# Optimization experiments

Measured on AMD Instinct MI355X. Metric: run time of the kernel, lower is better.

## Reference

```python
import jax, jax.numpy as jnp
import numpy as np

B, T, C = 2, 2048, 2048
HK, HV, DK, DV, KW = 16, 32, 128, 128, 4
KEY_DIM = HK * DK          # 2048
VAL_DIM = HV * DV          # 4096
QKV_DIM = 2 * KEY_DIM + VAL_DIM  # 8192
REPEAT = HV // HK
EPS = 1e-6


def setup_inputs() -> dict:
    key = jax.random.key(0)
    ks = jax.random.split(key, 12)
    s = 0.02
    return {
        "x": jax.random.normal(ks[0], (B, T, C), jnp.float32),
        "positions": jnp.arange(B * T, dtype=jnp.int64).reshape(B, T) % T,
        "W_qkv": jax.random.normal(ks[1], (QKV_DIM, C), jnp.float32) * s,
        "W_z": jax.random.normal(ks[2], (VAL_DIM, C), jnp.float32) * s,
        "W_b": jax.random.normal(ks[3], (HV, C), jnp.float32) * s,
        "W_a": jax.random.normal(ks[4], (HV, C), jnp.float32) * s,
        "conv_w": jax.random.normal(ks[5], (QKV_DIM, 1, KW), jnp.float32) * 0.3,
        "dt_bias": jnp.ones((HV,), jnp.float32),
        "A_log": jnp.log(jax.random.uniform(ks[6], (HV,), jnp.float32, 0.01, 16.0)),
        "norm_w": jnp.ones((DV,), jnp.float32),
        "W_out": jax.random.normal(ks[7], (C, VAL_DIM), jnp.float32) * s,
    }


def _forward(x, W_qkv, W_z, W_b, W_a, conv_w, dt_bias, A_log, norm_w, W_out):
    qkv = x @ W_qkv.T                                # [B,T,QKV_DIM]
    z = (x @ W_z.T).reshape(B, T, HV, DV)
    b = x @ W_b.T                                    # [B,T,HV]
    a = x @ W_a.T                                    # [B,T,HV]

    # depthwise causal conv1d (left pad KW-1), then SiLU
    qkv_c = jnp.transpose(qkv, (0, 2, 1))            # [B,QKV_DIM,T]
    qkv_c = jax.lax.conv_general_dilated(
        qkv_c, conv_w, window_strides=(1,), padding=[(KW - 1, 0)],
        dimension_numbers=("NCH", "OIH", "NCH"), feature_group_count=QKV_DIM)
    qkv = jax.nn.silu(jnp.transpose(qkv_c, (0, 2, 1)))

    q, k, v = jnp.split(qkv, [KEY_DIM, 2 * KEY_DIM], axis=-1)
    q = q.reshape(B, T, HK, DK)
    k = k.reshape(B, T, HK, DK)
    v = v.reshape(B, T, HV, DV)
    q = q / jnp.maximum(jnp.linalg.norm(q, axis=-1, keepdims=True), 1e-12)
    k = k / jnp.maximum(jnp.linalg.norm(k, axis=-1, keepdims=True), 1e-12)
    if REPEAT > 1:
        q = jnp.repeat(q, REPEAT, axis=2)            # [B,T,HV,DK]
        k = jnp.repeat(k, REPEAT, axis=2)

    beta = jax.nn.sigmoid(b)                         # [B,T,HV]
    g = -jnp.exp(A_log) * jax.nn.softplus(a + dt_bias)  # [B,T,HV]

    # gated delta-rule recurrence over time (lax.scan, time-major)
    def step(state, inp):
        g_t, beta_t, k_t, v_t, q_t = inp             # [B,HV], [B,HV], [B,HV,DK], [B,HV,DV], [B,HV,DK]
        state = jnp.exp(g_t)[..., None, None] * state \
            + beta_t[..., None, None] * (k_t[..., :, None] * v_t[..., None, :])
        out_t = jnp.einsum("bhk,bhkv->bhv", q_t, state)
        return state, out_t

    tm = lambda u: jnp.moveaxis(u, 1, 0)
    state0 = jnp.zeros((B, HV, DK, DV), x.dtype)
    _, out = jax.lax.scan(step, state0, (tm(g), tm(beta), tm(k), tm(v), tm(q)))
    out = jnp.moveaxis(out, 0, 1)                    # [B,T,HV,DV]

    # gated RMSNorm per head: RMSNorm(out) * silu(z)
    o = out.astype(jnp.float32)
    o = o * jax.lax.rsqrt(jnp.mean(o * o, axis=-1, keepdims=True) + EPS)
    o = (norm_w * o) * jax.nn.silu(z.astype(jnp.float32))
    o = o.astype(x.dtype).reshape(B, T, VAL_DIM)
    return o @ W_out.T                               # [B,T,C]


def reference(x, positions, W_qkv, W_z, W_b, W_a, conv_w, dt_bias, A_log, norm_w, W_out):
    del positions  # unused by the module's math
    return _forward(x, W_qkv, W_z, W_b, W_a, conv_w, dt_bias, A_log, norm_w, W_out)
```

## Files before the change

### kernel.cpp

```cpp
#include <hip/hip_runtime.h>

typedef unsigned short u16;
typedef unsigned int u32;
typedef __attribute__((ext_vector_type(8))) short short8;
typedef __attribute__((ext_vector_type(8))) _Float16 half8;
typedef __attribute__((ext_vector_type(4))) float f32x4;

#define NB 2
#define NT 2048
#define NC 2048
#define NHV 32
#define VALD 4096
#define NBT 4096
#define CL 64
#define NCH (NT / CL)

#define GL16(gp, lp) __builtin_amdgcn_global_load_lds( \
    (const __attribute__((address_space(1))) unsigned int*)(gp), \
    (__attribute__((address_space(3))) unsigned int*)(lp), 16, 0, 0)

static __device__ __forceinline__ float bf2f(u16 u) {
  union { u32 u; float f; } x; x.u = ((u32)u) << 16; return x.f;
}
static __device__ __forceinline__ u16 f2bf(float f) {
  union { float f; u32 u; } x; x.f = f;
  u32 r = x.u + 0x7fffu + ((x.u >> 16) & 1u);
  return (u16)(r >> 16);
}
static __device__ __forceinline__ u16 f2h(float f) {
  union { _Float16 h; u16 u; } c; c.h = (_Float16)f; return c.u;
}
static __device__ __forceinline__ float h2f(u16 u) {
  union { u16 u; _Float16 h; } c; c.u = u; return (float)c.h;
}
static __device__ __forceinline__ float sigm(float x) { return 1.0f / (1.0f + __expf(-x)); }
static __device__ __forceinline__ int ldsoff(int row, int c8) {
  return row * 48 + ((c8 ^ ((row >> 2) & 3)) << 3);
}

__global__ void k_sentinel(float* out) { out[0] = 1.0e6f; }

__global__ __launch_bounds__(256) void k_cvtx(const float* __restrict__ in, u16* __restrict__ hi,
                                              u16* __restrict__ lo, u16* __restrict__ h16, int n4) {
  int i = blockIdx.x * 256 + threadIdx.x;
  if (i >= n4) return;
  float4 v = ((const float4*)in)[i];
  ushort4 h, l, p;
  h.x = f2bf(v.x); l.x = f2bf(v.x - bf2f(h.x)); p.x = f2h(v.x);
  h.y = f2bf(v.y); l.y = f2bf(v.y - bf2f(h.y)); p.y = f2h(v.y);
  h.z = f2bf(v.z); l.z = f2bf(v.z - bf2f(h.z)); p.z = f2h(v.z);
  h.w = f2bf(v.w); l.w = f2bf(v.w - bf2f(h.w)); p.w = f2h(v.w);
  ((ushort4*)hi)[i] = h;
  ((ushort4*)lo)[i] = l;
  ((ushort4*)h16)[i] = p;
}

__global__ __launch_bounds__(256) void k_cvt16(const float* __restrict__ in, u16* __restrict__ out, int n4) {
  int i = blockIdx.x * 256 + threadIdx.x;
  if (i >= n4) return;
  float4 v = ((const float4*)in)[i];
  ushort4 o;
  o.x = f2h(v.x); o.y = f2h(v.y); o.z = f2h(v.z); o.w = f2h(v.w);
  ((ushort4*)out)[i] = o;
}

__global__ __launch_bounds__(256) void k_wba(const float* __restrict__ Wb, const float* __restrict__ Wa,
                                             u16* __restrict__ hi, u16* __restrict__ lo) {
  int i = blockIdx.x * 256 + threadIdx.x;
  int r = i >> 11, c = i & 2047;
  float v = 0.f;
  if (r < 32) v = Wb[r * 2048 + c];
  else if (r < 64) v = Wa[(r - 32) * 2048 + c];
  u16 h = f2bf(v);
  hi[i] = h;
  lo[i] = f2bf(v - bf2f(h));
}

__global__ __launch_bounds__(256) void k_gemm_bf3(const u16* __restrict__ Ahg, const u16* __restrict__ Alg,
                                                  const u16* __restrict__ Bhg, const u16* __restrict__ Blg,
                                                  float* __restrict__ C0, int M, int N, int K) {
  __shared__ __align__(16) u16 As_h[128 * 48];
  __shared__ __align__(16) u16 As_l[128 * 48];
  __shared__ __align__(16) u16 Bs_h[128 * 48];
  __shared__ __align__(16) u16 Bs_l[128 * 48];
  const int tid = threadIdx.x;
  const int lane = tid & 63, wave = tid >> 6;
  const int wr = wave >> 1, wc = wave & 1;
  const int l15 = lane & 15, l16 = lane >> 4;
  const int row0 = blockIdx.y * 128, col0 = blockIdx.x * 128;
  const int sr = tid >> 1, sk = (tid & 1) * 16;
  const int c0 = sk >> 3;
  const int w0 = ldsoff(sr, c0), w1 = ldsoff(sr, c0 + 1);
  f32x4 acc[4][4] = {};
  for (int k0 = 0; k0 < K; k0 += 32) {
    const size_t aoff = (size_t)(row0 + sr) * K + k0 + sk;
    const size_t boff = (size_t)(col0 + sr) * K + k0 + sk;
    *(short8*)&As_h[w0] = *(const short8*)&Ahg[aoff];
    *(short8*)&As_h[w1] = *(const short8*)&Ahg[aoff + 8];
    *(short8*)&As_l[w0] = *(const short8*)&Alg[aoff];
    *(short8*)&As_l[w1] = *(const short8*)&Alg[aoff + 8];
    *(short8*)&Bs_h[w0] = *(const short8*)&Bhg[boff];
    *(short8*)&Bs_h[w1] = *(const short8*)&Bhg[boff + 8];
    *(short8*)&Bs_l[w0] = *(const short8*)&Blg[boff];
    *(short8*)&Bs_l[w1] = *(const short8*)&Blg[boff + 8];
    __syncthreads();
    short8 ah[4], al[4], bh[4], bl[4];
#pragma unroll
    for (int mi = 0; mi < 4; ++mi) {
      int off = ldsoff(wr * 64 + mi * 16 + l15, l16);
      ah[mi] = *(short8*)&As_h[off];
      al[mi] = *(short8*)&As_l[off];
    }
#pragma unroll
    for (int ni = 0; ni < 4; ++ni) {
      int off = ldsoff(wc * 64 + ni * 16 + l15, l16);
      bh[ni] = *(short8*)&Bs_h[off];
      bl[ni] = *(short8*)&Bs_l[off];
    }
#pragma unroll
    for (int mi = 0; mi < 4; ++mi)
#pragma unroll
      for (int ni = 0; ni < 4; ++ni) {
        acc[mi][ni] = __builtin_amdgcn_mfma_f32_16x16x32_bf16(ah[mi], bh[ni], acc[mi][ni], 0, 0, 0);
        acc[mi][ni] = __builtin_amdgcn_mfma_f32_16x16x32_bf16(al[mi], bh[ni], acc[mi][ni], 0, 0, 0);
        acc[mi][ni] = __builtin_amdgcn_mfma_f32_16x16x32_bf16(ah[mi], bl[ni], acc[mi][ni], 0, 0, 0);
      }
    __syncthreads();
  }
#pragma unroll
  for (int mi = 0; mi < 4; ++mi)
#pragma unroll
    for (int ni = 0; ni < 4; ++ni) {
      int rr = row0 + wr * 64 + mi * 16 + l16 * 4;
      int cc = col0 + wc * 64 + ni * 16 + l15;
#pragma unroll
      for (int i = 0; i < 4; ++i)
        C0[(size_t)(rr + i) * N + cc] = acc[mi][ni][i];
    }
}

template <int MODE>
__global__ __launch_bounds__(256) void k_gemm16(const u16* __restrict__ Ag, const u16* __restrict__ Bg,
                                                void* __restrict__ C0, int M, int N, int K,
                                                const u16* __restrict__ e0, const float* __restrict__ e1,
                                                const float* __restrict__ e2) {
  __shared__ __align__(16) u16 As[2 * 128 * 64];
  __shared__ __align__(16) u16 Bs[2 * 128 * 64];
  const int tid = threadIdx.x;
  const int lane = tid & 63, wave = tid >> 6;
  const int wr = wave >> 1, wc = wave & 1;
  const int l15 = lane & 15, l16 = lane >> 4;
  const int qx = gridDim.x >> 3;
  const int swz = ((int)blockIdx.x & 7) * qx + ((int)blockIdx.x >> 3);
  const int nbx = N >> 7;
  const int row0 = (swz / nbx) * 128, col0 = (swz % nbx) * 128;
  u32 gA[4], gB[4], lofs[4];
#pragma unroll
  for (int i = 0; i < 4; ++i) {
    int o = wave * 2048 + i * 512 + lane * 8;
    int row = o >> 6;
    int cg = ((lane & 7) ^ (row & 7)) * 8;
    gA[i] = (u32)(row0 + row) * (u32)K + cg;
    gB[i] = (u32)(col0 + row) * (u32)K + cg;
    lofs[i] = (u32)(wave * 2048 + i * 512);
  }
  f32x4 acc[4][4] = {};
  const int NTILE = K >> 6;
#pragma unroll
  for (int i = 0; i < 4; ++i) {
    GL16(Ag + gA[i], &As[lofs[i]]);
    GL16(Bg + gB[i], &Bs[lofs[i]]);
  }
  for (int t = 0; t < NTILE; ++t) {
    const u32 cb = (u32)(t & 1) * 8192;
    __syncthreads();
    if (t + 1 < NTILE) {
      const u32 nb = cb ^ 8192;
      const int kn = (t + 1) << 6;
#pragma unroll
      for (int i = 0; i < 4; ++i) {
        GL16(Ag + gA[i] + kn, &As[nb + lofs[i]]);
        GL16(Bg + gB[i] + kn, &Bs[nb + lofs[i]]);
      }
    }
#pragma unroll
    for (int kk = 0; kk < 2; ++kk) {
      half8 a[4], b[4];
#pragma unroll
      for (int mi = 0; mi < 4; ++mi) {
        int row = wr * 64 + mi * 16 + l15;
        a[mi] = *(half8*)&As[cb + row * 64 + (((kk * 4 + l16) ^ (l15 & 7)) << 3)];
      }
#pragma unroll
      for (int ni = 0; ni < 4; ++ni) {
        int row = wc * 64 + ni * 16 + l15;
        b[ni] = *(half8*)&Bs[cb + row * 64 + (((kk * 4 + l16) ^ (l15 & 7)) << 3)];
      }
#pragma unroll
      for (int mi = 0; mi < 4; ++mi)
#pragma unroll
        for (int ni = 0; ni < 4; ++ni)
          acc[mi][ni] = __builtin_amdgcn_mfma_f32_16x16x32_f16(a[mi], b[ni], acc[mi][ni], 0, 0, 0);
    }
  }
#pragma unroll
  for (int mi = 0; mi < 4; ++mi) {
#pragma unroll
    for (int ni = 0; ni < 4; ++ni) {
      int rr = row0 + wr * 64 + mi * 16 + l16 * 4;
      int cc = col0 + wc * 64 + ni * 16 + l15;
#pragma unroll
      for (int i = 0; i < 4; ++i) {
        float v = acc[mi][ni][i];
        size_t idx = (size_t)(rr + i) * N + cc;
        if constexpr (MODE == 0) {
          ((float*)C0)[idx] = v;
        } else if constexpr (MODE == 1) {
          ((u16*)C0)[idx] = f2h(v);
        } else {
          float zs = v * sigm(v);
          float o = h2f(e0[idx]) * e1[(size_t)(rr + i) * 32 + (cc >> 7)] * e2[cc & 127] * zs;
          ((u16*)C0)[idx] = f2h(o);
        }
      }
    }
  }
}

__global__ __launch_bounds__(256) void k_bg(const float* __restrict__ ba, const float* __restrict__ dt_bias,
                                            const float* __restrict__ A_log, float* __restrict__ beta_t,
                                            float* __restrict__ g_t) {
  int i = blockIdx.x * 256 + threadIdx.x;
  int bt = i >> 5, h = i & 31;
  float bv = ba[(size_t)bt * 128 + h];
  float av = ba[(size_t)bt * 128 + 32 + h];
  beta_t[h * 4096 + bt] = sigm(bv);
  float xx = av + dt_bias[h];
  float sp = (xx > 20.f) ? xx : log1pf(__expf(xx));
  g_t[h * 4096 + bt] = -__expf(A_log[h]) * sp;
}

__global__ __launch_bounds__(256) void k_convqk(const u16* __restrict__ qkraw, const float* __restrict__ cw,
                                                u16* __restrict__ qkn) {
  __shared__ float sval[4096];
  __shared__ float snrm[32];
  const int tid = threadIdx.x;
  const int bt = blockIdx.x;
  const int b = bt >> 11, t = bt & 2047;
  for (int i = 0; i < 16; ++i) {
    int c = i * 256 + tid;
    float acc = 0.f;
#pragma unroll
    for (int j = 0; j < 4; ++j) {
      int ts = t - 3 + j;
      if (ts >= 0) acc += cw[c * 4 + j] * h2f(qkraw[(size_t)(b * 2048 + ts) * 4096 + c]);
    }
    sval[c] = acc * sigm(acc);
  }
  __syncthreads();
  {
    int gidx = tid >> 3, s = tid & 7;
    float ss = 0.f;
#pragma unroll
    for (int i2 = 0; i2 < 16; ++i2) { float v = sval[gidx * 128 + s * 16 + i2]; ss += v * v; }
    ss += __shfl_xor(ss, 1); ss += __shfl_xor(ss, 2); ss += __shfl_xor(ss, 4);
    if (s == 0) snrm[gidx] = 1.0f / fmaxf(sqrtf(ss), 1e-12f);
  }
  __syncthreads();
  for (int i = 0; i < 16; ++i) {
    int c = i * 256 + tid;
    qkn[(size_t)bt * 4096 + c] = f2h(sval[c] * snrm[c >> 7]);
  }
}

__global__ __launch_bounds__(512, 4) void k_scanc(const u16* __restrict__ qk16, const u16* __restrict__ v16,
                                                  const float* __restrict__ cw,
                                                  const float* __restrict__ beta_t, const float* __restrict__ g_t,
                                                  u16* __restrict__ outr) {
  __shared__ __align__(16) u16 Qs[64][136], Ks[64][136];
  __shared__ __align__(16) u16 Vs[32][72];
  __shared__ __align__(16) u16 SIs[64][72];
  __shared__ __align__(16) u16 SH[2][32][132];
  __shared__ u16 rv16[67][36];
  __shared__ float garr[2][64], barr[2][64], warr[2][64], earr[2][64];
  __shared__ float sdt[2];

  const int tid = threadIdx.x;
  const int lane = tid & 63, wv = tid >> 6;
  const int l15 = lane & 15, l16 = lane >> 4;
  const int dq = blockIdx.x & 3, h = (blockIdx.x >> 2) & 31, b = blockIdx.x >> 7;
  const int bT = b * 2048;
  const int hk = h >> 1;
  const int dvl = tid & 31;
  const int vch = h * 128 + dq * 32;
  const float4 cwv = *(const float4*)&cw[(4096 + vch + dvl) * 4];
  const int mblk = wv & 3, nh = wv >> 2;
  const int m0 = mblk * 16;
  const int sr = tid >> 3, d0 = (tid & 7) * 16;
  const int r0v = tid >> 5;

  for (int i = tid; i < 2 * 32 * 132; i += 512) ((u16*)SH)[i] = 0;
  f32x4 st[2] = {};

  short8 pq[2], pk[2];
  u16 pv[5];
  float pgv, pbv;
  auto LOADQK = [&](int t0) {
    const size_t base = (size_t)(bT + t0 + sr) * 4096 + hk * 128 + d0;
    pq[0] = *(const short8*)&qk16[base];        pq[1] = *(const short8*)&qk16[base + 8];
    pk[0] = *(const short8*)&qk16[base + 2048]; pk[1] = *(const short8*)&qk16[base + 2056];
  };
  auto LOADV = [&](int t0) {
#pragma unroll
    for (int i = 0; i < 5; ++i) {
      int r = r0v + i * 16;
      int tr = t0 - 3 + r;
      pv[i] = (r < 67 && tr >= 0) ? v16[(size_t)(bT + tr) * 4096 + vch + dvl] : (u16)0;
    }
  };
  auto CUMSUM = [&](float gv, float bv, int buf) {
    float cum = gv;
#pragma unroll
    for (int off = 1; off < 64; off <<= 1) {
      float o = __shfl_up(cum, off);
      if (lane >= off) cum += o;
    }
    float tot = __shfl(cum, 63);
    garr[buf][lane] = cum;
    earr[buf][lane] = __expf(cum);
    warr[buf][lane] = __expf(tot - cum) * bv;
    barr[buf][lane] = bv;
    if (lane == 0) sdt[buf] = __expf(tot);
  };

  LOADQK(0);
  LOADV(0);
  if (wv == 0) {
    float gv = g_t[h * 4096 + bT + lane];
    float bv = beta_t[h * 4096 + bT + lane];
    CUMSUM(gv, bv, 0);
  }

  for (int ch = 0; ch < NCH; ++ch) {
    const int t0 = ch * CL;
    const int p = ch & 1;
    *(short8*)&Qs[sr][d0] = pq[0]; *(short8*)&Qs[sr][d0 + 8] = pq[1];
    *(short8*)&Ks[sr][d0] = pk[0]; *(short8*)&Ks[sr][d0 + 8] = pk[1];
#pragma unroll
    for (int i = 0; i < 5; ++i) {
      int r = r0v + i * 16;
      if (r < 67) rv16[r][dvl] = pv[i];
    }
    __syncthreads();
    if (ch + 1 < NCH) {
      LOADQK(t0 + CL);
      LOADV(t0 + CL);
      if (wv == 0) {
        pgv = g_t[h * 4096 + bT + t0 + CL + lane];
        pbv = beta_t[h * 4096 + bT + t0 + CL + lane];
      }
    }
    {
      int tl = tid >> 5;
#pragma unroll
      for (int rr = 0; rr < 4; ++rr) {
        int t = rr * 16 + tl;
        float a = cwv.x * h2f(rv16[t][dvl]) + cwv.y * h2f(rv16[t + 1][dvl]) +
                  cwv.z * h2f(rv16[t + 2][dvl]) + cwv.w * h2f(rv16[t + 3][dvl]);
        a = a * sigm(a);
        Vs[dvl][t] = f2h(a);
      }
    }
    half8 a[4];
#pragma unroll
    for (int kk = 0; kk < 4; ++kk) a[kk] = *(half8*)&Qs[m0 + l15][l16 * 8 + kk * 32];
#pragma unroll
    for (int j = 0; j < 2; ++j) {
      int n = nh * 2 + j;
      f32x4 a4 = {};
#pragma unroll
      for (int kk = 0; kk < 4; ++kk) {
        half8 b8 = *(half8*)&Ks[n * 16 + l15][l16 * 8 + kk * 32];
        a4 = __builtin_amdgcn_mfma_f32_16x16x32_f16(a[kk], b8, a4, 0, 0, 0);
      }
      int col = n * 16 + l15;
      float gc = garr[p][col], bc = barr[p][col];
#pragma unroll
      for (int i = 0; i < 4; ++i) {
        int row = m0 + l16 * 4 + i;
        float cval = (col <= row) ? __expf(garr[p][row] - gc) * bc * a4[i] : 0.f;
        SIs[row][col] = f2h(cval);
      }
    }
    __syncthreads();
    f32x4 ao = {};
#pragma unroll
    for (int kk = 0; kk < 4; ++kk) {
      half8 s8 = *(half8*)&SH[p][nh * 16 + l15][l16 * 8 + kk * 32];
      ao = __builtin_amdgcn_mfma_f32_16x16x32_f16(a[kk], s8, ao, 0, 0, 0);
    }
#pragma unroll
    for (int i = 0; i < 4; ++i) ao[i] *= earr[p][m0 + l16 * 4 + i];
#pragma unroll
    for (int kk = 0; kk < 2; ++kk) {
      half8 asi = *(half8*)&SIs[m0 + l15][l16 * 8 + kk * 32];
      half8 bv8 = *(half8*)&Vs[nh * 16 + l15][l16 * 8 + kk * 32];
      ao = __builtin_amdgcn_mfma_f32_16x16x32_f16(asi, bv8, ao, 0, 0, 0);
    }
#pragma unroll
    for (int i = 0; i < 4; ++i)
      outr[(size_t)(bT + t0 + m0 + l16 * 4 + i) * 4096 + vch + nh * 16 + l15] = f2h(ao[i]);
    const float sd = sdt[p];
#pragma unroll
    for (int m = 0; m < 2; ++m)
#pragma unroll
      for (int i = 0; i < 4; ++i) st[m][i] *= sd;
#pragma unroll
    for (int kk = 0; kk < 2; ++kk) {
      half8 bw;
      {
        int dk = wv * 16 + l15;
#pragma unroll
        for (int e = 0; e < 8; ++e) {
          int s = l16 * 8 + e + kk * 32;
          bw[e] = (_Float16)(h2f(Ks[s][dk]) * warr[p][s]);
        }
      }
#pragma unroll
      for (int m = 0; m < 2; ++m) {
        half8 av = *(half8*)&Vs[m * 16 + l15][l16 * 8 + kk * 32];
        st[m] = __builtin_amdgcn_mfma_f32_16x16x32_f16(av, bw, st[m], 0, 0, 0);
      }
    }
#pragma unroll
    for (int m = 0; m < 2; ++m)
#pragma unroll
      for (int i = 0; i < 4; ++i)
        SH[p ^ 1][m * 16 + l16 * 4 + i][wv * 16 + l15] = f2h(st[m][i]);
    if (wv == 0 && ch + 1 < NCH) CUMSUM(pgv, pbv, p ^ 1);
    __syncthreads();
  }
}

__global__ __launch_bounds__(256) void k_rms(const u16* __restrict__ outr, float* __restrict__ rms) {
  int pair = blockIdx.x * 4 + (threadIdx.x >> 6);
  int lane = threadIdx.x & 63;
  u32 pv = *(const u32*)&outr[(size_t)pair * 128 + lane * 2];
  float v0 = h2f((u16)pv), v1 = h2f((u16)(pv >> 16));
  float ss = v0 * v0 + v1 * v1;
#pragma unroll
  for (int m = 1; m < 64; m <<= 1) ss += __shfl_xor(ss, m);
  if (lane == 0) rms[pair] = rsqrtf(ss * (1.0f / 128.0f) + 1e-6f);
}

extern "C" void kernel_launch(void* const* d_in, const int* in_sizes, int n_in,
                              void* d_out, int out_size, void* d_ws, size_t ws_size,
                              hipStream_t stream) {
  const float* x = (const float*)d_in[0];
  const float* W_qkv = (const float*)d_in[2];
  const float* W_z = (const float*)d_in[3];
  const float* W_b = (const float*)d_in[4];
  const float* W_a = (const float*)d_in[5];
  const float* conv_w = (const float*)d_in[6];
  const float* dt_bias = (const float*)d_in[7];
  const float* A_log = (const float*)d_in[8];
  const float* norm_w = (const float*)d_in[9];
  const float* W_out = (const float*)d_in[10];
  float* out = (float*)d_out;

  const size_t MB = 1ull << 20;
  const size_t need = 192 * MB + 3 * (size_t)NBT * 32 * 4;
  if (ws_size < need) {
    k_sentinel<<<1, 1, 0, stream>>>(out);
    return;
  }
  char* ws = (char*)d_ws;
  u16* xh = (u16*)ws;
  u16* xl = (u16*)(ws + 16 * MB);
  u16* xh16 = (u16*)(ws + 32 * MB);
  u16* wz16 = (u16*)(ws + 48 * MB);
  u16* qkB16 = (u16*)(ws + 64 * MB);
  u16* wout16 = (u16*)(ws + 64 * MB);
  u16* qkA16 = (u16*)(ws + 96 * MB);
  u16* om16 = (u16*)(ws + 96 * MB);
  u16* wsh16 = (u16*)(ws + 128 * MB);
  u16* outr16 = (u16*)(ws + 128 * MB);
  u16* v16 = (u16*)(ws + 160 * MB);
  u16* wbah = (u16*)(ws + 160 * MB);
  u16* wbal = (u16*)(ws + 160 * MB + 512 * 1024);
  float* babuf = (float*)(ws + 161 * MB);
  float* beta_t = (float*)(ws + 192 * MB);
  float* g_t = beta_t + (size_t)NBT * 32;
  float* rmsb = g_t + (size_t)NBT * 32;

  const int N4X = NBT * NC / 4;
  k_cvtx<<<N4X / 256, 256, 0, stream>>>(x, xh, xl, xh16, N4X);
  k_cvt16<<<2 * N4X / 256, 256, 0, stream>>>(W_qkv, wsh16, 2 * N4X);
  k_cvt16<<<N4X / 256, 256, 0, stream>>>(W_z, wz16, N4X);
  k_wba<<<128 * NC / 256, 256, 0, stream>>>(W_b, W_a, wbah, wbal);
  k_gemm_bf3<<<dim3(1, NBT / 128), 256, 0, stream>>>(xh, xl, wbah, wbal, babuf, NBT, 128, NC);
  k_bg<<<NBT * 32 / 256, 256, 0, stream>>>(babuf, dt_bias, A_log, beta_t, g_t);

  k_gemm16<1><<<(NBT / 128) * (4096 / 128), 256, 0, stream>>>(xh16, wsh16, qkA16, NBT, 4096, NC,
                                                              nullptr, nullptr, nullptr);
  k_convqk<<<NBT, 256, 0, stream>>>(qkA16, conv_w, qkB16);

  k_gemm16<1><<<(NBT / 128) * (4096 / 128), 256, 0, stream>>>(xh16, wsh16 + (size_t)4096 * NC, v16,
                                                              NBT, 4096, NC, nullptr, nullptr, nullptr);

  k_scanc<<<256, 512, 0, stream>>>(qkB16, v16, conv_w, beta_t, g_t, outr16);
  k_rms<<<NBT * NHV / 4, 256, 0, stream>>>(outr16, rmsb);

  k_gemm16<2><<<(NBT / 128) * (VALD / 128), 256, 0, stream>>>(xh16, wz16, om16, NBT, VALD, NC,
                                                              outr16, rmsb, norm_w);

  k_cvt16<<<N4X / 256, 256, 0, stream>>>(W_out, wout16, N4X);
  k_gemm16<0><<<(NBT / 128) * (NC / 128), 256, 0, stream>>>(om16, wout16, out, NBT, NC, VALD,
                                                            nullptr, nullptr, nullptr);
}
```

Measured before the change: 644.2 us.

## Split-K the b/a projection GEMM and merge QK and V GEMMs into one launch

The small b/a projection GEMM (N=128) previously ran on only 32 blocks. It now splits K four ways into separate partial buffers, and k_bg sums the four partials. The q/k and v projection GEMMs are merged into a single 8192-column launch with a new epilogue mode that routes each column tile to the qk or v buffer. This raises occupancy and removes a launch, at the cost of extra partial-buffer traffic, and it relies on the babuf4 region being large enough for four copies.

```diff
diff --git a/kernel.cpp b/kernel.cpp
--- a/kernel.cpp
+++ b/kernel.cpp
@@ -87,12 +87,16 @@
   const int lane = tid & 63, wave = tid >> 6;
   const int wr = wave >> 1, wc = wave & 1;
   const int l15 = lane & 15, l16 = lane >> 4;
-  const int row0 = blockIdx.y * 128, col0 = blockIdx.x * 128;
+  const int kc = blockIdx.x;
+  const int Kc = K >> 2;
+  const int kbase = kc * Kc;
+  const int row0 = blockIdx.y * 128, col0 = 0;
+  float* Cp = C0 + (size_t)kc * M * N;
   const int sr = tid >> 1, sk = (tid & 1) * 16;
   const int c0 = sk >> 3;
   const int w0 = ldsoff(sr, c0), w1 = ldsoff(sr, c0 + 1);
   f32x4 acc[4][4] = {};
-  for (int k0 = 0; k0 < K; k0 += 32) {
+  for (int k0 = kbase; k0 < kbase + Kc; k0 += 32) {
     const size_t aoff = (size_t)(row0 + sr) * K + k0 + sk;
     const size_t boff = (size_t)(col0 + sr) * K + k0 + sk;
     *(short8*)&As_h[w0] = *(const short8*)&Ahg[aoff];
@@ -135,13 +139,14 @@
       int cc = col0 + wc * 64 + ni * 16 + l15;
 #pragma unroll
       for (int i = 0; i < 4; ++i)
-        C0[(size_t)(rr + i) * N + cc] = acc[mi][ni][i];
+        Cp[(size_t)(rr + i) * N + cc] = acc[mi][ni][i];
     }
 }
 
 template <int MODE>
 __global__ __launch_bounds__(256) void k_gemm16(const u16* __restrict__ Ag, const u16* __restrict__ Bg,
-                                                void* __restrict__ C0, int M, int N, int K,
+                                                void* __restrict__ C0, void* __restrict__ C1,
+                                                int M, int N, int K,
                                                 const u16* __restrict__ e0, const float* __restrict__ e1,
                                                 const float* __restrict__ e2) {
   __shared__ __align__(16) u16 As[2 * 128 * 64];
@@ -203,6 +208,12 @@
           acc[mi][ni] = __builtin_amdgcn_mfma_f32_16x16x32_f16(a[mi], b[ni], acc[mi][ni], 0, 0, 0);
     }
   }
+  u16* Cs = nullptr;
+  int cbase = col0;
+  if constexpr (MODE == 3) {
+    Cs = (col0 < 4096) ? (u16*)C0 : (u16*)C1;
+    cbase = col0 & 4095;
+  }
 #pragma unroll
   for (int mi = 0; mi < 4; ++mi) {
 #pragma unroll
@@ -212,15 +223,18 @@
 #pragma unroll
       for (int i = 0; i < 4; ++i) {
         float v = acc[mi][ni][i];
-        size_t idx = (size_t)(rr + i) * N + cc;
         if constexpr (MODE == 0) {
-          ((float*)C0)[idx] = v;
+          ((float*)C0)[(size_t)(rr + i) * N + cc] = v;
         } else if constexpr (MODE == 1) {
-          ((u16*)C0)[idx] = f2h(v);
-        } else {
+          ((u16*)C0)[(size_t)(rr + i) * N + cc] = f2h(v);
+        } else if constexpr (MODE == 2) {
+          size_t idx = (size_t)(rr + i) * N + cc;
           float zs = v * sigm(v);
           float o = h2f(e0[idx]) * e1[(size_t)(rr + i) * 32 + (cc >> 7)] * e2[cc & 127] * zs;
           ((u16*)C0)[idx] = f2h(o);
+        } else {
+          int c2 = cbase + wc * 64 + ni * 16 + l15;
+          Cs[(size_t)(rr + i) * 4096 + c2] = f2h(v);
         }
       }
     }
@@ -232,8 +246,11 @@
                                             float* __restrict__ g_t) {
   int i = blockIdx.x * 256 + threadIdx.x;
   int bt = i >> 5, h = i & 31;
-  float bv = ba[(size_t)bt * 128 + h];
-  float av = ba[(size_t)bt * 128 + 32 + h];
+  const size_t P = (size_t)4096 * 128;
+  float bv = ba[(size_t)bt * 128 + h] + ba[P + (size_t)bt * 128 + h] +
+             ba[2 * P + (size_t)bt * 128 + h] + ba[3 * P + (size_t)bt * 128 + h];
+  float av = ba[(size_t)bt * 128 + 32 + h] + ba[P + (size_t)bt * 128 + 32 + h] +
+             ba[2 * P + (size_t)bt * 128 + 32 + h] + ba[3 * P + (size_t)bt * 128 + 32 + h];
   beta_t[h * 4096 + bt] = sigm(bv);
   float xx = av + dt_bias[h];
   float sp = (xx > 20.f) ? xx : log1pf(__expf(xx));
@@ -488,7 +505,7 @@
   u16* v16 = (u16*)(ws + 160 * MB);
   u16* wbah = (u16*)(ws + 160 * MB);
   u16* wbal = (u16*)(ws + 160 * MB + 512 * 1024);
-  float* babuf = (float*)(ws + 161 * MB);
+  float* babuf4 = (float*)(ws + 161 * MB);
   float* beta_t = (float*)(ws + 192 * MB);
   float* g_t = beta_t + (size_t)NBT * 32;
   float* rmsb = g_t + (size_t)NBT * 32;
@@ -498,23 +515,20 @@
   k_cvt16<<<2 * N4X / 256, 256, 0, stream>>>(W_qkv, wsh16, 2 * N4X);
   k_cvt16<<<N4X / 256, 256, 0, stream>>>(W_z, wz16, N4X);
   k_wba<<<128 * NC / 256, 256, 0, stream>>>(W_b, W_a, wbah, wbal);
-  k_gemm_bf3<<<dim3(1, NBT / 128), 256, 0, stream>>>(xh, xl, wbah, wbal, babuf, NBT, 128, NC);
-  k_bg<<<NBT * 32 / 256, 256, 0, stream>>>(babuf, dt_bias, A_log, beta_t, g_t);
-
-  k_gemm16<1><<<(NBT / 128) * (4096 / 128), 256, 0, stream>>>(xh16, wsh16, qkA16, NBT, 4096, NC,
-                                                              nullptr, nullptr, nullptr);
+  k_gemm_bf3<<<dim3(4, NBT / 128), 256, 0, stream>>>(xh, xl, wbah, wbal, babuf4, NBT, 128, NC);
+  k_bg<<<NBT * 32 / 256, 256, 0, stream>>>(babuf4, dt_bias, A_log, beta_t, g_t);
+
+  k_gemm16<3><<<(NBT / 128) * (8192 / 128), 256, 0, stream>>>(xh16, wsh16, qkA16, v16,
+                                                              NBT, 8192, NC, nullptr, nullptr, nullptr);
   k_convqk<<<NBT, 256, 0, stream>>>(qkA16, conv_w, qkB16);
-
-  k_gemm16<1><<<(NBT / 128) * (4096 / 128), 256, 0, stream>>>(xh16, wsh16 + (size_t)4096 * NC, v16,
-                                                              NBT, 4096, NC, nullptr, nullptr, nullptr);
 
   k_scanc<<<256, 512, 0, stream>>>(qkB16, v16, conv_w, beta_t, g_t, outr16);
   k_rms<<<NBT * NHV / 4, 256, 0, stream>>>(outr16, rmsb);
 
-  k_gemm16<2><<<(NBT / 128) * (VALD / 128), 256, 0, stream>>>(xh16, wz16, om16, NBT, VALD, NC,
+  k_gemm16<2><<<(NBT / 128) * (VALD / 128), 256, 0, stream>>>(xh16, wz16, om16, nullptr, NBT, VALD, NC,
                                                               outr16, rmsb, norm_w);
 
   k_cvt16<<<N4X / 256, 256, 0, stream>>>(W_out, wout16, N4X);
-  k_gemm16<0><<<(NBT / 128) * (NC / 128), 256, 0, stream>>>(om16, wout16, out, NBT, NC, VALD,
+  k_gemm16<0><<<(NBT / 128) * (NC / 128), 256, 0, stream>>>(om16, wout16, out, nullptr, NBT, NC, VALD,
                                                             nullptr, nullptr, nullptr);
 }
```

Measured after the change: 588.9 us. -8.6%, faster.
